# Kernel optimization log

Measured on AMD Instinct MI355X. Metric: run time of the kernel, lower is better.

Reference implementation:

```python
import jax, jax.numpy as jnp
import numpy as np
from jax.ops import segment_sum

N = 100000   # nodes
E = 1600000  # edges
F = 128      # node feature dim
H = 128      # hidden dim
FE = 16      # edge feature dim
G = 256      # num graphs
EPS = 1e-5   # batch-norm eps


def setup_inputs() -> dict:
    key = jax.random.key(0)
    ks = jax.random.split(key, 16)
    s = 0.05
    return {
        "x": jax.random.normal(ks[0], (N, F), jnp.float32),
        "edge_index": jax.random.randint(ks[1], (2, E), 0, N, dtype=jnp.int32),
        "edge_attr": jax.random.normal(ks[2], (E, FE), jnp.float32),
        "batch_idx": jnp.sort(jax.random.randint(ks[3], (N,), 0, G, dtype=jnp.int32)),
        # GCN layer 1
        "W_g1": jax.random.normal(ks[4], (F, H), jnp.float32) * s,
        "b_g1": jnp.zeros((H,), jnp.float32),
        "gamma1": jnp.ones((H,), jnp.float32),
        "beta1": jnp.zeros((H,), jnp.float32),
        # GCN layer 2
        "W_g2": jax.random.normal(ks[5], (H, H), jnp.float32) * s,
        "b_g2": jnp.zeros((H,), jnp.float32),
        "gamma2": jnp.ones((H,), jnp.float32),
        "beta2": jnp.zeros((H,), jnp.float32),
        # edge encoder MLP
        "W_e1": jax.random.normal(ks[6], (FE, H), jnp.float32) * s,
        "b_e1": jnp.zeros((H,), jnp.float32),
        "W_e2": jax.random.normal(ks[7], (H, H), jnp.float32) * s,
        "b_e2": jnp.zeros((H,), jnp.float32),
    }


def _gcn_bn_relu(x, src, dst, W, b, gamma, beta):
    """GCNConv (sym-normalized, self-loops) + BatchNorm1d (batch stats) + ReLU."""
    h = x @ W                                             # [N, H]
    ones = jnp.ones((E,), h.dtype)
    deg = segment_sum(ones, dst, num_segments=N) + 1.0    # self-loop degree
    dinv = jax.lax.rsqrt(deg)                             # [N]
    norm = dinv[src] * dinv[dst]                          # [E]
    agg = segment_sum(h[src] * norm[:, None], dst, num_segments=N)
    out = agg + h * (dinv * dinv)[:, None] + b            # self-loop + bias
    mu = out.mean(axis=0)
    var = out.var(axis=0)
    out = (out - mu) * jax.lax.rsqrt(var + EPS) * gamma + beta
    return jax.nn.relu(out)


def reference(x, edge_index, edge_attr, batch_idx, W_g1, b_g1, gamma1, beta1,
              W_g2, b_g2, gamma2, beta2, W_e1, b_e1, W_e2, b_e2):
    src, dst = edge_index[0], edge_index[1]
    h = _gcn_bn_relu(x, src, dst, W_g1, b_g1, gamma1, beta1)
    h = _gcn_bn_relu(h, src, dst, W_g2, b_g2, gamma2, beta2)

    # global mean pool over nodes per graph
    node_cnt = segment_sum(jnp.ones((N,), h.dtype), batch_idx, num_segments=G)
    graph_repr = segment_sum(h, batch_idx, num_segments=G) / jnp.maximum(node_cnt, 1.0)[:, None]

    # edge encoder MLP + per-graph edge mean (vectorized version of the loop)
    e = jax.nn.relu(edge_attr @ W_e1 + b_e1) @ W_e2 + b_e2   # [E, H]
    edge_batch = batch_idx[src]                              # [E]
    edge_cnt = segment_sum(jnp.ones((E,), e.dtype), edge_batch, num_segments=G)
    edge_sum = segment_sum(e, edge_batch, num_segments=G)
    edge_repr = jnp.where(edge_cnt[:, None] > 0, edge_sum / jnp.maximum(edge_cnt, 1.0)[:, None], 0.0)

    return graph_repr + edge_repr  # [G, H]
```

## Files before the change

### kernel.cpp

```cpp
#include <hip/hip_runtime.h>
#include <cstdint>

__device__ inline unsigned int bfpack2(float a, float b) {
  unsigned int ua = __float_as_uint(a), ub = __float_as_uint(b);
  ua += 0x7FFFu + ((ua >> 16) & 1u);
  ub += 0x7FFFu + ((ub >> 16) & 1u);
  return (ua >> 16) | (ub & 0xFFFF0000u);
}
__device__ inline float bflo(unsigned int u) { return __uint_as_float(u << 16); }
__device__ inline float bfhi(unsigned int u) { return __uint_as_float(u & 0xFFFF0000u); }

__global__ __launch_bounds__(256) void pre_kernel(const int* __restrict__ src,
                                                  const int* __restrict__ dst,
                                                  int* __restrict__ deg,
                                                  int* __restrict__ deg2, int nE) {
  int e = blockIdx.x * 256 + threadIdx.x;
  if (e < nE) {
    atomicAdd(&deg[dst[e]], 1);
    atomicAdd(&deg2[src[e]], 1);
  }
}

__global__ __launch_bounds__(256) void scanA_kernel(const int* __restrict__ deg,
                                                    const int* __restrict__ deg2,
                                                    int* __restrict__ rp,
                                                    int* __restrict__ rp2,
                                                    int* __restrict__ part,
                                                    int* __restrict__ part2,
                                                    int n, int nb) {
  __shared__ int sh[256];
  int b = blockIdx.x, t = threadIdx.x;
  const int* d = (b < nb) ? deg : deg2;
  int* r = (b < nb) ? rp : rp2;
  int* p = (b < nb) ? part : part2;
  int pad = (b < nb) ? 1 : 0;
  int bb = (b < nb) ? b : b - nb;
  int base = bb * 1024 + t * 4;
  int v0 = (base + 0 < n) ? d[base + 0] : 0;
  int v1 = (base + 1 < n) ? d[base + 1] : 0;
  int v2 = (base + 2 < n) ? d[base + 2] : 0;
  int v3 = (base + 3 < n) ? d[base + 3] : 0;
  if (pad) {
    v0 = (v0 + 7) & ~7; v1 = (v1 + 7) & ~7;
    v2 = (v2 + 7) & ~7; v3 = (v3 + 7) & ~7;
  }
  int ts = v0 + v1 + v2 + v3;
  sh[t] = ts;
  __syncthreads();
  for (int off = 1; off < 256; off <<= 1) {
    int x = (t >= off) ? sh[t - off] : 0;
    __syncthreads();
    sh[t] += x;
    __syncthreads();
  }
  int excl = sh[t] - ts;
  if (t == 255) p[bb] = sh[255];
  if (base + 0 < n) r[base + 0] = excl;
  if (base + 1 < n) r[base + 1] = excl + v0;
  if (base + 2 < n) r[base + 2] = excl + v0 + v1;
  if (base + 3 < n) r[base + 3] = excl + v0 + v1 + v2;
}

__global__ void scanB_kernel(int* part, int* part2, int* rp, int* rp2, int nb, int n) {
  if (threadIdx.x == 0) {
    int* p = (blockIdx.x == 0) ? part : part2;
    int* r = (blockIdx.x == 0) ? rp : rp2;
    int run = 0;
    for (int i = 0; i < nb; ++i) { int v = p[i]; p[i] = run; run += v; }
    r[n] = run;
  }
}

__global__ __launch_bounds__(256) void scanC_kernel(int* __restrict__ rp,
                                                    int* __restrict__ rp2,
                                                    const int* __restrict__ part,
                                                    const int* __restrict__ part2,
                                                    int* __restrict__ cursor,
                                                    int* __restrict__ cursor2,
                                                    const int* __restrict__ deg,
                                                    float* __restrict__ dinv, int n) {
  int i = blockIdx.x * 256 + threadIdx.x;
  if (i < n) {
    int v = rp[i] + part[i >> 10];
    rp[i] = v;
    cursor[i] = v;
    dinv[i] = rsqrtf((float)deg[i] + 1.0f);
  } else if (i < 2 * n) {
    int j = i - n;
    int v = rp2[j] + part2[j >> 10];
    rp2[j] = v;
    cursor2[j] = v;
  }
}

__global__ __launch_bounds__(256) void placepad_kernel(const int* __restrict__ src,
                                                       const int* __restrict__ dst,
                                                       const int* __restrict__ batch,
                                                       const float* __restrict__ dinv,
                                                       int* __restrict__ cursor,
                                                       int* __restrict__ cursor2,
                                                       int2* __restrict__ swv,
                                                       unsigned int* __restrict__ epk,
                                                       const int* __restrict__ rp,
                                                       const int* __restrict__ deg,
                                                       int nE, int nN) {
  int t = blockIdx.x * 256 + threadIdx.x;
  if (t < nE) {
    int s = src[t];
    int d = dst[t];
    int p1 = atomicAdd(&cursor[d], 1);
    int2 sw; sw.x = s; sw.y = __float_as_int(dinv[s] * dinv[d]);
    swv[p1] = sw;
    int g = batch[s];
    int p2 = atomicAdd(&cursor2[s], 1);
    epk[p2] = ((unsigned int)g << 21) | (unsigned int)t;
  } else if (t < nE + nN) {
    int i = t - nE;
    int b = rp[i] + deg[i], e = rp[i + 1];
    int2 z; z.x = i; z.y = 0;
    for (int k = b; k < e; ++k) swv[k] = z;
  }
}

template <bool FUSED>
__global__ __launch_bounds__(256) void gemm128_kernel(const float* __restrict__ A,
                                                      const float* __restrict__ W,
                                                      const float* __restrict__ scale,
                                                      const float* __restrict__ shift,
                                                      unsigned int* __restrict__ hpk2,
                                                      int nrows) {
  extern __shared__ float lds[];
  float* Ws = lds;
  float* xs = lds + 128 * 128;
  const int t = threadIdx.x;
  for (int i = t; i < (128 * 128) / 4; i += 256)
    reinterpret_cast<float4*>(Ws)[i] = reinterpret_cast<const float4*>(W)[i];
  const int wave = t >> 6, lane = t & 63;
  const size_t sbase = (size_t)(lane >> 3) * (size_t)nrows * 8 + (lane & 7);
  for (int rb = blockIdx.x * 16; rb < nrows; rb += gridDim.x * 16) {
    int nr = min(16, nrows - rb);
    __syncthreads();
    for (int i = t; i < nr * 32; i += 256) {
      float4 v = reinterpret_cast<const float4*>(A + (size_t)rb * 128)[i];
      if (FUSED) {
        float4 sc4 = reinterpret_cast<const float4*>(scale)[i & 31];
        float4 sh4 = reinterpret_cast<const float4*>(shift)[i & 31];
        v.x = fmaxf(fmaf(v.x, sc4.x, sh4.x), 0.f);
        v.y = fmaxf(fmaf(v.y, sc4.y, sh4.y), 0.f);
        v.z = fmaxf(fmaf(v.z, sc4.z, sh4.z), 0.f);
        v.w = fmaxf(fmaf(v.w, sc4.w, sh4.w), 0.f);
      }
      reinterpret_cast<float4*>(xs)[i] = v;
    }
    __syncthreads();
    float acc[4][2] = {{0.f, 0.f}, {0.f, 0.f}, {0.f, 0.f}, {0.f, 0.f}};
    const float* xw = xs + wave * 4 * 128;
#pragma unroll 4
    for (int k = 0; k < 128; ++k) {
      float w0 = Ws[k * 128 + lane];
      float w1 = Ws[k * 128 + 64 + lane];
#pragma unroll
      for (int r = 0; r < 4; ++r) {
        float a = xw[r * 128 + k];
        acc[r][0] = fmaf(a, w0, acc[r][0]);
        acc[r][1] = fmaf(a, w1, acc[r][1]);
      }
    }
#pragma unroll
    for (int r = 0; r < 4; ++r) {
      int row = rb + wave * 4 + r;
      if (row < nrows)
        hpk2[sbase + (size_t)row * 8] = bfpack2(acc[r][0], acc[r][1]);
    }
  }
}

__global__ __launch_bounds__(256) void spmm8_kernel(const unsigned int* __restrict__ hpk2,
                                                    const float* __restrict__ dinv,
                                                    const int* __restrict__ rp,
                                                    const int2* __restrict__ swv,
                                                    const float* __restrict__ bias,
                                                    float* __restrict__ outp,
                                                    float* __restrict__ bnsum,
                                                    float* __restrict__ bnsq, int nN) {
  const int lane = threadIdx.x & 63;
  const int ch = lane & 7;
  const int es = lane >> 3;
  const int slice = blockIdx.x & 7;
  const unsigned int* hs = hpk2 + (size_t)slice * (size_t)nN * 8;
  const int cb = slice * 8;
  const int wib = (int)(blockIdx.x >> 3) * 4 + (int)(threadIdx.x >> 6);
  const int nws = (int)(gridDim.x >> 3) * 4;
  const unsigned long long* swq = reinterpret_cast<const unsigned long long*>(swv);
  float b0 = bias[cb + ch], b1 = bias[64 + cb + ch];
  float s0 = 0.f, s1 = 0.f, q0 = 0.f, q1 = 0.f;
  for (int n = wib; n < nN; n += nws) {
    const int beg = rp[n], end = rp[n + 1];
    float a0 = 0.f, a1 = 0.f, c0 = 0.f, c1 = 0.f;
    int j = beg;
    for (; j + 8 < end; j += 16) {
      unsigned long long v0 = __builtin_nontemporal_load(swq + j + es);
      unsigned long long v1 = __builtin_nontemporal_load(swq + j + 8 + es);
      int sA = (int)(unsigned int)v0;
      int sB = (int)(unsigned int)v1;
      float wA = __uint_as_float((unsigned int)(v0 >> 32));
      float wB = __uint_as_float((unsigned int)(v1 >> 32));
      unsigned int pA = hs[(size_t)sA * 8 + ch];
      unsigned int pB = hs[(size_t)sB * 8 + ch];
      a0 = fmaf(wA, bflo(pA), a0); a1 = fmaf(wA, bfhi(pA), a1);
      c0 = fmaf(wB, bflo(pB), c0); c1 = fmaf(wB, bfhi(pB), c1);
    }
    if (j < end) {
      unsigned long long v0 = __builtin_nontemporal_load(swq + j + es);
      int sA = (int)(unsigned int)v0;
      float wA = __uint_as_float((unsigned int)(v0 >> 32));
      unsigned int pA = hs[(size_t)sA * 8 + ch];
      a0 = fmaf(wA, bflo(pA), a0); a1 = fmaf(wA, bfhi(pA), a1);
    }
    a0 += c0; a1 += c1;
    a0 += __shfl_xor(a0, 8);  a1 += __shfl_xor(a1, 8);
    a0 += __shfl_xor(a0, 16); a1 += __shfl_xor(a1, 16);
    a0 += __shfl_xor(a0, 32); a1 += __shfl_xor(a1, 32);
    if (es == 0) {
      float dn = dinv[n];
      float sw = dn * dn;
      unsigned int pn = hs[(size_t)n * 8 + ch];
      float o0 = fmaf(bflo(pn), sw, a0) + b0;
      float o1 = fmaf(bfhi(pn), sw, a1) + b1;
      __builtin_nontemporal_store(o0, &outp[(size_t)n * 128 + cb + ch]);
      __builtin_nontemporal_store(o1, &outp[(size_t)n * 128 + 64 + cb + ch]);
      s0 += o0; s1 += o1;
      q0 = fmaf(o0, o0, q0); q1 = fmaf(o1, o1, q1);
    }
  }
  if (es == 0) {
    atomicAdd(&bnsum[cb + ch], s0);
    atomicAdd(&bnsum[64 + cb + ch], s1);
    atomicAdd(&bnsq[cb + ch], q0);
    atomicAdd(&bnsq[64 + cb + ch], q1);
  }
}

__global__ void bnfin_kernel(const float* __restrict__ sum, const float* __restrict__ sq,
                             const float* __restrict__ gamma, const float* __restrict__ beta,
                             float* __restrict__ scale, float* __restrict__ shift,
                             float invN) {
  int c = threadIdx.x;
  float mu = sum[c] * invN;
  float var = sq[c] * invN - mu * mu;
  float sc = gamma[c] * rsqrtf(var + 1e-5f);
  scale[c] = sc;
  shift[c] = beta[c] - mu * sc;
}

__global__ __launch_bounds__(256) void pool_kernel(const float* __restrict__ h,
                                                   const int* __restrict__ batch,
                                                   const float* __restrict__ scale,
                                                   const float* __restrict__ shift,
                                                   float* __restrict__ gsum,
                                                   float* __restrict__ gcnt,
                                                   int nN, int chunk) {
  const int lane = threadIdx.x & 63;
  const int wid = (blockIdx.x * blockDim.x + threadIdx.x) >> 6;
  int beg = wid * chunk;
  if (beg >= nN) return;
  int end = min(nN, beg + chunk);
  const int c2 = 2 * lane;
  float2 sc2 = *reinterpret_cast<const float2*>(scale + c2);
  float2 sh2 = *reinterpret_cast<const float2*>(shift + c2);
  int cur = -1;
  float a0 = 0.f, a1 = 0.f, cnt = 0.f;
  for (int n = beg; n < end; ++n) {
    int g = batch[n];
    if (g != cur) {
      if (cur >= 0) {
        atomicAdd(&gsum[cur * 128 + c2], a0);
        atomicAdd(&gsum[cur * 128 + c2 + 1], a1);
        if (lane == 0) atomicAdd(&gcnt[cur], cnt);
      }
      cur = g; a0 = 0.f; a1 = 0.f; cnt = 0.f;
    }
    float2 v = *reinterpret_cast<const float2*>(h + (size_t)n * 128 + c2);
    a0 += fmaxf(fmaf(v.x, sc2.x, sh2.x), 0.f);
    a1 += fmaxf(fmaf(v.y, sc2.y, sh2.y), 0.f);
    cnt += 1.f;
  }
  if (cur >= 0) {
    atomicAdd(&gsum[cur * 128 + c2], a0);
    atomicAdd(&gsum[cur * 128 + c2 + 1], a1);
    if (lane == 0) atomicAdd(&gcnt[cur], cnt);
  }
}

__global__ __launch_bounds__(256) void edge2_kernel(const float* __restrict__ ea,
                                                    const unsigned int* __restrict__ epk,
                                                    const float* __restrict__ We1,
                                                    const float* __restrict__ be1,
                                                    float* __restrict__ esum,
                                                    float* __restrict__ ecnt,
                                                    int nE, int chunk) {
  const int lane = threadIdx.x & 63;
  const int wid = (blockIdx.x * 256 + threadIdx.x) >> 6;
  int beg = wid * chunk;
  if (beg >= nE) return;
  int end = min(nE, beg + chunk);
  float w0[16], w1[16];
#pragma unroll
  for (int k = 0; k < 16; ++k) {
    w0[k] = We1[k * 128 + lane];
    w1[k] = We1[k * 128 + 64 + lane];
  }
  float b0 = be1[lane], b1 = be1[64 + lane];
  int cur = -1;
  float a0 = 0.f, a1 = 0.f, cnt = 0.f;
  for (int j = beg; j < end; ++j) {
    unsigned int pk = epk[j];
    int g = (int)(pk >> 21);
    int e = (int)(pk & 0x1FFFFFu);
    if (g != cur) {
      if (cur >= 0) {
        atomicAdd(&esum[cur * 128 + lane], a0);
        atomicAdd(&esum[cur * 128 + 64 + lane], a1);
        if (lane == 0) atomicAdd(&ecnt[cur], cnt);
      }
      cur = g; a0 = 0.f; a1 = 0.f; cnt = 0.f;
    }
    const float4* eap = reinterpret_cast<const float4*>(ea + (size_t)e * 16);
    float4 t0 = eap[0], t1 = eap[1], t2 = eap[2], t3 = eap[3];
    float u0 = b0, u1 = b1;
    u0 = fmaf(t0.x, w0[0], u0);  u1 = fmaf(t0.x, w1[0], u1);
    u0 = fmaf(t0.y, w0[1], u0);  u1 = fmaf(t0.y, w1[1], u1);
    u0 = fmaf(t0.z, w0[2], u0);  u1 = fmaf(t0.z, w1[2], u1);
    u0 = fmaf(t0.w, w0[3], u0);  u1 = fmaf(t0.w, w1[3], u1);
    u0 = fmaf(t1.x, w0[4], u0);  u1 = fmaf(t1.x, w1[4], u1);
    u0 = fmaf(t1.y, w0[5], u0);  u1 = fmaf(t1.y, w1[5], u1);
    u0 = fmaf(t1.z, w0[6], u0);  u1 = fmaf(t1.z, w1[6], u1);
    u0 = fmaf(t1.w, w0[7], u0);  u1 = fmaf(t1.w, w1[7], u1);
    u0 = fmaf(t2.x, w0[8], u0);  u1 = fmaf(t2.x, w1[8], u1);
    u0 = fmaf(t2.y, w0[9], u0);  u1 = fmaf(t2.y, w1[9], u1);
    u0 = fmaf(t2.z, w0[10], u0); u1 = fmaf(t2.z, w1[10], u1);
    u0 = fmaf(t2.w, w0[11], u0); u1 = fmaf(t2.w, w1[11], u1);
    u0 = fmaf(t3.x, w0[12], u0); u1 = fmaf(t3.x, w1[12], u1);
    u0 = fmaf(t3.y, w0[13], u0); u1 = fmaf(t3.y, w1[13], u1);
    u0 = fmaf(t3.z, w0[14], u0); u1 = fmaf(t3.z, w1[14], u1);
    u0 = fmaf(t3.w, w0[15], u0); u1 = fmaf(t3.w, w1[15], u1);
    a0 += fmaxf(u0, 0.f);
    a1 += fmaxf(u1, 0.f);
    cnt += 1.f;
  }
  if (cur >= 0) {
    atomicAdd(&esum[cur * 128 + lane], a0);
    atomicAdd(&esum[cur * 128 + 64 + lane], a1);
    if (lane == 0) atomicAdd(&ecnt[cur], cnt);
  }
}

__global__ __launch_bounds__(128) void final_kernel(const float* __restrict__ gsum,
                                                    const float* __restrict__ gcnt,
                                                    const float* __restrict__ esum,
                                                    const float* __restrict__ ecnt,
                                                    const float* __restrict__ We2,
                                                    const float* __restrict__ be2,
                                                    float* __restrict__ out) {
  __shared__ float row[128];
  int g = blockIdx.x, c = threadIdx.x;
  row[c] = esum[g * 128 + c];
  __syncthreads();
  float acc = 0.f;
#pragma unroll 4
  for (int k = 0; k < 128; ++k) acc = fmaf(row[k], We2[k * 128 + c], acc);
  float ce = ecnt[g];
  float er = (ce > 0.f) ? (acc / ce + be2[c]) : 0.f;
  float cn = gcnt[g];
  float gr = gsum[g * 128 + c] / fmaxf(cn, 1.f);
  out[g * 128 + c] = gr + er;
}

extern "C" void kernel_launch(void* const* d_in, const int* in_sizes, int n_in,
                              void* d_out, int out_size, void* d_ws, size_t ws_size,
                              hipStream_t stream) {
  const float* x    = (const float*)d_in[0];
  const int*   ei   = (const int*)d_in[1];
  const float* ea   = (const float*)d_in[2];
  const int*   bidx = (const int*)d_in[3];
  const float* Wg1  = (const float*)d_in[4];
  const float* bg1  = (const float*)d_in[5];
  const float* gm1  = (const float*)d_in[6];
  const float* bt1  = (const float*)d_in[7];
  const float* Wg2  = (const float*)d_in[8];
  const float* bg2  = (const float*)d_in[9];
  const float* gm2  = (const float*)d_in[10];
  const float* bt2  = (const float*)d_in[11];
  const float* We1  = (const float*)d_in[12];
  const float* be1  = (const float*)d_in[13];
  const float* We2  = (const float*)d_in[14];
  const float* be2  = (const float*)d_in[15];
  float* out = (float*)d_out;

  const int N = in_sizes[3];
  const int E = in_sizes[1] / 2;
  const int G = out_size / 128;
  const int* srcp = ei;
  const int* dstp = ei + E;
  const int Epad = E + 8 * N;

  char* w = (char*)d_ws;
  auto alloc = [&](size_t b) {
    char* p = w;
    w += (b + 15) & ~(size_t)15;
    return p;
  };
  float* bufB    = (float*)alloc((size_t)N * 128 * 4);
  unsigned int* hpk2 = (unsigned int*)alloc((size_t)N * 64 * 4);
  int2*  swv     = (int2*)alloc((size_t)Epad * 8);
  unsigned int* epk = (unsigned int*)alloc((size_t)E * 4);
  int*   rp      = (int*)alloc((size_t)(N + 1) * 4);
  int*   rp2     = (int*)alloc((size_t)(N + 1) * 4);
  int*   cursor  = (int*)alloc((size_t)N * 4);
  int*   cursor2 = (int*)alloc((size_t)N * 4);
  float* dinv    = (float*)alloc((size_t)N * 4);
  char* zbase = w;
  int*   deg  = (int*)alloc((size_t)N * 4);
  int*   deg2 = (int*)alloc((size_t)N * 4);
  float* bs1  = (float*)alloc(512);
  float* bq1  = (float*)alloc(512);
  float* bs2  = (float*)alloc(512);
  float* bq2  = (float*)alloc(512);
  float* gsum = (float*)alloc((size_t)G * 128 * 4);
  float* gcnt = (float*)alloc((size_t)G * 4);
  float* esum = (float*)alloc((size_t)G * 128 * 4);
  float* ecnt = (float*)alloc((size_t)G * 4);
  int*   part  = (int*)alloc(4096);
  int*   part2 = (int*)alloc(4096);
  size_t zbytes = (size_t)(w - zbase);
  float* sc1 = (float*)alloc(512);
  float* sh1 = (float*)alloc(512);
  float* sc2 = (float*)alloc(512);
  float* sh2 = (float*)alloc(512);

  hipMemsetAsync(zbase, 0, zbytes, stream);

  (void)hipFuncSetAttribute((const void*)gemm128_kernel<false>,
                            hipFuncAttributeMaxDynamicSharedMemorySize, 73728);
  (void)hipFuncSetAttribute((const void*)gemm128_kernel<true>,
                            hipFuncAttributeMaxDynamicSharedMemorySize, 73728);

  pre_kernel<<<(E + 255) / 256, 256, 0, stream>>>(srcp, dstp, deg, deg2, E);
  int nb = (N + 1023) / 1024;
  scanA_kernel<<<2 * nb, 256, 0, stream>>>(deg, deg2, rp, rp2, part, part2, N, nb);
  scanB_kernel<<<2, 64, 0, stream>>>(part, part2, rp, rp2, nb, N);
  scanC_kernel<<<(2 * N + 255) / 256, 256, 0, stream>>>(rp, rp2, part, part2, cursor,
                                                        cursor2, deg, dinv, N);
  placepad_kernel<<<(E + N + 255) / 256, 256, 0, stream>>>(srcp, dstp, bidx, dinv, cursor,
                                                           cursor2, swv, epk, rp, deg, E, N);

  gemm128_kernel<false><<<512, 256, 73728, stream>>>(x, Wg1, nullptr, nullptr, hpk2, N);
  spmm8_kernel<<<2048, 256, 0, stream>>>(hpk2, dinv, rp, swv, bg1, bufB, bs1, bq1, N);
  bnfin_kernel<<<1, 128, 0, stream>>>(bs1, bq1, gm1, bt1, sc1, sh1, 1.0f / (float)N);

  gemm128_kernel<true><<<512, 256, 73728, stream>>>(bufB, Wg2, sc1, sh1, hpk2, N);
  spmm8_kernel<<<2048, 256, 0, stream>>>(hpk2, dinv, rp, swv, bg2, bufB, bs2, bq2, N);
  bnfin_kernel<<<1, 128, 0, stream>>>(bs2, bq2, gm2, bt2, sc2, sh2, 1.0f / (float)N);

  int nwp = (2048 * 256) / 64;
  int chunkN = (N + nwp - 1) / nwp;
  pool_kernel<<<2048, 256, 0, stream>>>(bufB, bidx, sc2, sh2, gsum, gcnt, N, chunkN);
  int nwe = (2048 * 256) / 64;
  int chunkE = (E + nwe - 1) / nwe;
  edge2_kernel<<<2048, 256, 0, stream>>>(ea, epk, We1, be1, esum, ecnt, E, chunkE);
  final_kernel<<<G, 128, 0, stream>>>(gsum, gcnt, esum, ecnt, We2, be2, out);
}
```

Before: 1.336 ms.

## Drop source-sorted edge CSR; accumulate edge means in LDS; pair nodes in SpMM

Removes the second CSR build (source degrees, second scan, cursor2, epk placement) that only served the edge encoder. The edge encoder now streams edges in their original order, looks up each edge's graph through src and batch, and accumulates per-graph sums in a full 256x128 LDS table using shared atomics. Each block writes that table to a per-block partial buffer that aliases hpk2, and final_kernel reduces the 256 partials. Separately, the SpMM kernel processes two nodes per wave iteration to expose more independent gathers, at the cost of more registers and uneven tail handling.

After: 1.969 ms. 47.3% more time.

```diff
diff --git a/kernel.cpp b/kernel.cpp
--- a/kernel.cpp
+++ b/kernel.cpp
@@ -10,40 +10,24 @@
 __device__ inline float bflo(unsigned int u) { return __uint_as_float(u << 16); }
 __device__ inline float bfhi(unsigned int u) { return __uint_as_float(u & 0xFFFF0000u); }
 
-__global__ __launch_bounds__(256) void pre_kernel(const int* __restrict__ src,
-                                                  const int* __restrict__ dst,
-                                                  int* __restrict__ deg,
-                                                  int* __restrict__ deg2, int nE) {
+__global__ __launch_bounds__(256) void pre_kernel(const int* __restrict__ dst,
+                                                  int* __restrict__ deg, int nE) {
   int e = blockIdx.x * 256 + threadIdx.x;
-  if (e < nE) {
-    atomicAdd(&deg[dst[e]], 1);
-    atomicAdd(&deg2[src[e]], 1);
-  }
+  if (e < nE) atomicAdd(&deg[dst[e]], 1);
 }
 
 __global__ __launch_bounds__(256) void scanA_kernel(const int* __restrict__ deg,
-                                                    const int* __restrict__ deg2,
                                                     int* __restrict__ rp,
-                                                    int* __restrict__ rp2,
-                                                    int* __restrict__ part,
-                                                    int* __restrict__ part2,
-                                                    int n, int nb) {
+                                                    int* __restrict__ part, int n) {
   __shared__ int sh[256];
   int b = blockIdx.x, t = threadIdx.x;
-  const int* d = (b < nb) ? deg : deg2;
-  int* r = (b < nb) ? rp : rp2;
-  int* p = (b < nb) ? part : part2;
-  int pad = (b < nb) ? 1 : 0;
-  int bb = (b < nb) ? b : b - nb;
-  int base = bb * 1024 + t * 4;
-  int v0 = (base + 0 < n) ? d[base + 0] : 0;
-  int v1 = (base + 1 < n) ? d[base + 1] : 0;
-  int v2 = (base + 2 < n) ? d[base + 2] : 0;
-  int v3 = (base + 3 < n) ? d[base + 3] : 0;
-  if (pad) {
-    v0 = (v0 + 7) & ~7; v1 = (v1 + 7) & ~7;
-    v2 = (v2 + 7) & ~7; v3 = (v3 + 7) & ~7;
-  }
+  int base = b * 1024 + t * 4;
+  int v0 = (base + 0 < n) ? deg[base + 0] : 0;
+  int v1 = (base + 1 < n) ? deg[base + 1] : 0;
+  int v2 = (base + 2 < n) ? deg[base + 2] : 0;
+  int v3 = (base + 3 < n) ? deg[base + 3] : 0;
+  v0 = (v0 + 7) & ~7; v1 = (v1 + 7) & ~7;
+  v2 = (v2 + 7) & ~7; v3 = (v3 + 7) & ~7;
   int ts = v0 + v1 + v2 + v3;
   sh[t] = ts;
   __syncthreads();
@@ -54,29 +38,24 @@
     __syncthreads();
   }
   int excl = sh[t] - ts;
-  if (t == 255) p[bb] = sh[255];
-  if (base + 0 < n) r[base + 0] = excl;
-  if (base + 1 < n) r[base + 1] = excl + v0;
-  if (base + 2 < n) r[base + 2] = excl + v0 + v1;
-  if (base + 3 < n) r[base + 3] = excl + v0 + v1 + v2;
-}
-
-__global__ void scanB_kernel(int* part, int* part2, int* rp, int* rp2, int nb, int n) {
-  if (threadIdx.x == 0) {
-    int* p = (blockIdx.x == 0) ? part : part2;
-    int* r = (blockIdx.x == 0) ? rp : rp2;
+  if (t == 255) part[b] = sh[255];
+  if (base + 0 < n) rp[base + 0] = excl;
+  if (base + 1 < n) rp[base + 1] = excl + v0;
+  if (base + 2 < n) rp[base + 2] = excl + v0 + v1;
+  if (base + 3 < n) rp[base + 3] = excl + v0 + v1 + v2;
+}
+
+__global__ void scanB_kernel(int* part, int* rp, int nb, int n) {
+  if (blockIdx.x == 0 && threadIdx.x == 0) {
     int run = 0;
-    for (int i = 0; i < nb; ++i) { int v = p[i]; p[i] = run; run += v; }
-    r[n] = run;
+    for (int i = 0; i < nb; ++i) { int v = part[i]; part[i] = run; run += v; }
+    rp[n] = run;
   }
 }
 
 __global__ __launch_bounds__(256) void scanC_kernel(int* __restrict__ rp,
-                                                    int* __restrict__ rp2,
                                                     const int* __restrict__ part,
-                                                    const int* __restrict__ part2,
                                                     int* __restrict__ cursor,
-                                                    int* __restrict__ cursor2,
                                                     const int* __restrict__ deg,
                                                     float* __restrict__ dinv, int n) {
   int i = blockIdx.x * 256 + threadIdx.x;
@@ -85,22 +64,14 @@
     rp[i] = v;
     cursor[i] = v;
     dinv[i] = rsqrtf((float)deg[i] + 1.0f);
-  } else if (i < 2 * n) {
-    int j = i - n;
-    int v = rp2[j] + part2[j >> 10];
-    rp2[j] = v;
-    cursor2[j] = v;
   }
 }
 
 __global__ __launch_bounds__(256) void placepad_kernel(const int* __restrict__ src,
                                                        const int* __restrict__ dst,
-                                                       const int* __restrict__ batch,
                                                        const float* __restrict__ dinv,
                                                        int* __restrict__ cursor,
-                                                       int* __restrict__ cursor2,
                                                        int2* __restrict__ swv,
-                                                       unsigned int* __restrict__ epk,
                                                        const int* __restrict__ rp,
                                                        const int* __restrict__ deg,
                                                        int nE, int nN) {
@@ -111,9 +82,6 @@
     int p1 = atomicAdd(&cursor[d], 1);
     int2 sw; sw.x = s; sw.y = __float_as_int(dinv[s] * dinv[d]);
     swv[p1] = sw;
-    int g = batch[s];
-    int p2 = atomicAdd(&cursor2[s], 1);
-    epk[p2] = ((unsigned int)g << 21) | (unsigned int)t;
   } else if (t < nE + nN) {
     int i = t - nE;
     int b = rp[i] + deg[i], e = rp[i + 1];
@@ -194,45 +162,81 @@
   const unsigned long long* swq = reinterpret_cast<const unsigned long long*>(swv);
   float b0 = bias[cb + ch], b1 = bias[64 + cb + ch];
   float s0 = 0.f, s1 = 0.f, q0 = 0.f, q1 = 0.f;
-  for (int n = wib; n < nN; n += nws) {
-    const int beg = rp[n], end = rp[n + 1];
-    float a0 = 0.f, a1 = 0.f, c0 = 0.f, c1 = 0.f;
-    int j = beg;
-    for (; j + 8 < end; j += 16) {
-      unsigned long long v0 = __builtin_nontemporal_load(swq + j + es);
-      unsigned long long v1 = __builtin_nontemporal_load(swq + j + 8 + es);
-      int sA = (int)(unsigned int)v0;
-      int sB = (int)(unsigned int)v1;
-      float wA = __uint_as_float((unsigned int)(v0 >> 32));
-      float wB = __uint_as_float((unsigned int)(v1 >> 32));
-      unsigned int pA = hs[(size_t)sA * 8 + ch];
-      unsigned int pB = hs[(size_t)sB * 8 + ch];
-      a0 = fmaf(wA, bflo(pA), a0); a1 = fmaf(wA, bfhi(pA), a1);
-      c0 = fmaf(wB, bflo(pB), c0); c1 = fmaf(wB, bfhi(pB), c1);
-    }
-    if (j < end) {
-      unsigned long long v0 = __builtin_nontemporal_load(swq + j + es);
-      int sA = (int)(unsigned int)v0;
-      float wA = __uint_as_float((unsigned int)(v0 >> 32));
-      unsigned int pA = hs[(size_t)sA * 8 + ch];
-      a0 = fmaf(wA, bflo(pA), a0); a1 = fmaf(wA, bfhi(pA), a1);
-    }
-    a0 += c0; a1 += c1;
-    a0 += __shfl_xor(a0, 8);  a1 += __shfl_xor(a1, 8);
-    a0 += __shfl_xor(a0, 16); a1 += __shfl_xor(a1, 16);
-    a0 += __shfl_xor(a0, 32); a1 += __shfl_xor(a1, 32);
+  const int half = (nN + 1) >> 1;
+
+#define SPMM_CHUNK(J, ACC0, ACC1)                                         \
+  {                                                                       \
+    unsigned long long v_ = __builtin_nontemporal_load(swq + (J) + es);   \
+    unsigned int pp_ = hs[(size_t)(unsigned int)v_ * 8 + ch];             \
+    float ww_ = __uint_as_float((unsigned int)(v_ >> 32));                \
+    ACC0 = fmaf(ww_, bflo(pp_), ACC0);                                    \
+    ACC1 = fmaf(ww_, bfhi(pp_), ACC1);                                    \
+  }
+
+  for (int p = wib; p < half; p += nws) {
+    const int n0 = p;
+    const int n1 = p + half;
+    const bool has1 = n1 < nN;
+    int j0 = rp[n0];
+    const int end0 = rp[n0 + 1];
+    int j1 = 0, end1 = 0;
+    if (has1) { j1 = rp[n1]; end1 = rp[n1 + 1]; }
+    float a00 = 0.f, a01 = 0.f, b00 = 0.f, b01 = 0.f;
+    float a10 = 0.f, a11 = 0.f, b10 = 0.f, b11 = 0.f;
+    while (j0 + 8 < end0 && j1 + 8 < end1) {
+      SPMM_CHUNK(j0, a00, a01);
+      SPMM_CHUNK(j0 + 8, b00, b01);
+      SPMM_CHUNK(j1, a10, a11);
+      SPMM_CHUNK(j1 + 8, b10, b11);
+      j0 += 16; j1 += 16;
+    }
+    while (j0 + 8 < end0) {
+      SPMM_CHUNK(j0, a00, a01);
+      SPMM_CHUNK(j0 + 8, b00, b01);
+      j0 += 16;
+    }
+    if (j0 < end0) SPMM_CHUNK(j0, a00, a01);
+    while (j1 + 8 < end1) {
+      SPMM_CHUNK(j1, a10, a11);
+      SPMM_CHUNK(j1 + 8, b10, b11);
+      j1 += 16;
+    }
+    if (j1 < end1) SPMM_CHUNK(j1, a10, a11);
+
+    a00 += b00; a01 += b01;
+    a10 += b10; a11 += b11;
+    a00 += __shfl_xor(a00, 8);  a01 += __shfl_xor(a01, 8);
+    a10 += __shfl_xor(a10, 8);  a11 += __shfl_xor(a11, 8);
+    a00 += __shfl_xor(a00, 16); a01 += __shfl_xor(a01, 16);
+    a10 += __shfl_xor(a10, 16); a11 += __shfl_xor(a11, 16);
+    a00 += __shfl_xor(a00, 32); a01 += __shfl_xor(a01, 32);
+    a10 += __shfl_xor(a10, 32); a11 += __shfl_xor(a11, 32);
     if (es == 0) {
-      float dn = dinv[n];
-      float sw = dn * dn;
-      unsigned int pn = hs[(size_t)n * 8 + ch];
-      float o0 = fmaf(bflo(pn), sw, a0) + b0;
-      float o1 = fmaf(bfhi(pn), sw, a1) + b1;
-      __builtin_nontemporal_store(o0, &outp[(size_t)n * 128 + cb + ch]);
-      __builtin_nontemporal_store(o1, &outp[(size_t)n * 128 + 64 + cb + ch]);
-      s0 += o0; s1 += o1;
-      q0 = fmaf(o0, o0, q0); q1 = fmaf(o1, o1, q1);
-    }
-  }
+      {
+        float dn = dinv[n0];
+        float sw = dn * dn;
+        unsigned int pn = hs[(size_t)n0 * 8 + ch];
+        float o0 = fmaf(bflo(pn), sw, a00) + b0;
+        float o1 = fmaf(bfhi(pn), sw, a01) + b1;
+        __builtin_nontemporal_store(o0, &outp[(size_t)n0 * 128 + cb + ch]);
+        __builtin_nontemporal_store(o1, &outp[(size_t)n0 * 128 + 64 + cb + ch]);
+        s0 += o0; s1 += o1;
+        q0 = fmaf(o0, o0, q0); q1 = fmaf(o1, o1, q1);
+      }
+      if (has1) {
+        float dn = dinv[n1];
+        float sw = dn * dn;
+        unsigned int pn = hs[(size_t)n1 * 8 + ch];
+        float o0 = fmaf(bflo(pn), sw, a10) + b0;
+        float o1 = fmaf(bfhi(pn), sw, a11) + b1;
+        __builtin_nontemporal_store(o0, &outp[(size_t)n1 * 128 + cb + ch]);
+        __builtin_nontemporal_store(o1, &outp[(size_t)n1 * 128 + 64 + cb + ch]);
+        s0 += o0; s1 += o1;
+        q0 = fmaf(o0, o0, q0); q1 = fmaf(o1, o1, q1);
+      }
+    }
+  }
+#undef SPMM_CHUNK
   if (es == 0) {
     atomicAdd(&bnsum[cb + ch], s0);
     atomicAdd(&bnsum[64 + cb + ch], s1);
@@ -292,18 +296,18 @@
   }
 }
 
-__global__ __launch_bounds__(256) void edge2_kernel(const float* __restrict__ ea,
-                                                    const unsigned int* __restrict__ epk,
-                                                    const float* __restrict__ We1,
-                                                    const float* __restrict__ be1,
-                                                    float* __restrict__ esum,
-                                                    float* __restrict__ ecnt,
-                                                    int nE, int chunk) {
-  const int lane = threadIdx.x & 63;
-  const int wid = (blockIdx.x * 256 + threadIdx.x) >> 6;
-  int beg = wid * chunk;
-  if (beg >= nE) return;
-  int end = min(nE, beg + chunk);
+__global__ __launch_bounds__(1024) void edge3_kernel(const float* __restrict__ ea,
+                                                     const int* __restrict__ src,
+                                                     const int* __restrict__ batch,
+                                                     const float* __restrict__ We1,
+                                                     const float* __restrict__ be1,
+                                                     float* __restrict__ pb,
+                                                     int nE, int chunk) {
+  extern __shared__ float es[];
+  float* cs = es + 256 * 128;
+  const int t = threadIdx.x;
+  for (int i = t; i < 256 * 128 + 256; i += 1024) es[i] = 0.f;
+  const int lane = t & 63;
   float w0[16], w1[16];
 #pragma unroll
   for (int k = 0; k < 16; ++k) {
@@ -311,68 +315,86 @@
     w1[k] = We1[k * 128 + 64 + lane];
   }
   float b0 = be1[lane], b1 = be1[64 + lane];
-  int cur = -1;
-  float a0 = 0.f, a1 = 0.f, cnt = 0.f;
-  for (int j = beg; j < end; ++j) {
-    unsigned int pk = epk[j];
-    int g = (int)(pk >> 21);
-    int e = (int)(pk & 0x1FFFFFu);
-    if (g != cur) {
-      if (cur >= 0) {
-        atomicAdd(&esum[cur * 128 + lane], a0);
-        atomicAdd(&esum[cur * 128 + 64 + lane], a1);
-        if (lane == 0) atomicAdd(&ecnt[cur], cnt);
-      }
-      cur = g; a0 = 0.f; a1 = 0.f; cnt = 0.f;
-    }
-    const float4* eap = reinterpret_cast<const float4*>(ea + (size_t)e * 16);
-    float4 t0 = eap[0], t1 = eap[1], t2 = eap[2], t3 = eap[3];
-    float u0 = b0, u1 = b1;
-    u0 = fmaf(t0.x, w0[0], u0);  u1 = fmaf(t0.x, w1[0], u1);
-    u0 = fmaf(t0.y, w0[1], u0);  u1 = fmaf(t0.y, w1[1], u1);
-    u0 = fmaf(t0.z, w0[2], u0);  u1 = fmaf(t0.z, w1[2], u1);
-    u0 = fmaf(t0.w, w0[3], u0);  u1 = fmaf(t0.w, w1[3], u1);
-    u0 = fmaf(t1.x, w0[4], u0);  u1 = fmaf(t1.x, w1[4], u1);
-    u0 = fmaf(t1.y, w0[5], u0);  u1 = fmaf(t1.y, w1[5], u1);
-    u0 = fmaf(t1.z, w0[6], u0);  u1 = fmaf(t1.z, w1[6], u1);
-    u0 = fmaf(t1.w, w0[7], u0);  u1 = fmaf(t1.w, w1[7], u1);
-    u0 = fmaf(t2.x, w0[8], u0);  u1 = fmaf(t2.x, w1[8], u1);
-    u0 = fmaf(t2.y, w0[9], u0);  u1 = fmaf(t2.y, w1[9], u1);
-    u0 = fmaf(t2.z, w0[10], u0); u1 = fmaf(t2.z, w1[10], u1);
-    u0 = fmaf(t2.w, w0[11], u0); u1 = fmaf(t2.w, w1[11], u1);
-    u0 = fmaf(t3.x, w0[12], u0); u1 = fmaf(t3.x, w1[12], u1);
-    u0 = fmaf(t3.y, w0[13], u0); u1 = fmaf(t3.y, w1[13], u1);
-    u0 = fmaf(t3.z, w0[14], u0); u1 = fmaf(t3.z, w1[14], u1);
-    u0 = fmaf(t3.w, w0[15], u0); u1 = fmaf(t3.w, w1[15], u1);
-    a0 += fmaxf(u0, 0.f);
-    a1 += fmaxf(u1, 0.f);
-    cnt += 1.f;
-  }
-  if (cur >= 0) {
-    atomicAdd(&esum[cur * 128 + lane], a0);
-    atomicAdd(&esum[cur * 128 + 64 + lane], a1);
-    if (lane == 0) atomicAdd(&ecnt[cur], cnt);
-  }
+  __syncthreads();
+  const int wid = (blockIdx.x * 1024 + t) >> 6;
+  int beg = wid * chunk;
+  int end = min(nE, beg + chunk);
+  if (beg < end) {
+    int e = beg;
+    for (; e + 1 < end; e += 2) {
+      int s0 = src[e], s1 = src[e + 1];
+      int g0 = batch[s0], g1 = batch[s1];
+      const float4* p0 = reinterpret_cast<const float4*>(ea + (size_t)e * 16);
+      float4 A0 = p0[0], A1 = p0[1], A2 = p0[2], A3 = p0[3];
+      float4 B0 = p0[4], B1 = p0[5], B2 = p0[6], B3 = p0[7];
+      float av[16] = {A0.x, A0.y, A0.z, A0.w, A1.x, A1.y, A1.z, A1.w,
+                      A2.x, A2.y, A2.z, A2.w, A3.x, A3.y, A3.z, A3.w};
+      float bv[16] = {B0.x, B0.y, B0.z, B0.w, B1.x, B1.y, B1.z, B1.w,
+                      B2.x, B2.y, B2.z, B2.w, B3.x, B3.y, B3.z, B3.w};
+      float u0 = b0, u1 = b1, x0 = b0, x1 = b1;
+#pragma unroll
+      for (int k = 0; k < 16; ++k) {
+        u0 = fmaf(av[k], w0[k], u0);
+        u1 = fmaf(av[k], w1[k], u1);
+        x0 = fmaf(bv[k], w0[k], x0);
+        x1 = fmaf(bv[k], w1[k], x1);
+      }
+      u0 = fmaxf(u0, 0.f); u1 = fmaxf(u1, 0.f);
+      x0 = fmaxf(x0, 0.f); x1 = fmaxf(x1, 0.f);
+      atomicAdd(&es[g0 * 128 + lane], u0);
+      atomicAdd(&es[g0 * 128 + 64 + lane], u1);
+      atomicAdd(&es[g1 * 128 + lane], x0);
+      atomicAdd(&es[g1 * 128 + 64 + lane], x1);
+      if (lane == 0) {
+        atomicAdd(&cs[g0], 1.f);
+        atomicAdd(&cs[g1], 1.f);
+      }
+    }
+    if (e < end) {
+      int s0 = src[e];
+      int g0 = batch[s0];
+      const float4* p0 = reinterpret_cast<const float4*>(ea + (size_t)e * 16);
+      float4 A0 = p0[0], A1 = p0[1], A2 = p0[2], A3 = p0[3];
+      float av[16] = {A0.x, A0.y, A0.z, A0.w, A1.x, A1.y, A1.z, A1.w,
+                      A2.x, A2.y, A2.z, A2.w, A3.x, A3.y, A3.z, A3.w};
+      float u0 = b0, u1 = b1;
+#pragma unroll
+      for (int k = 0; k < 16; ++k) {
+        u0 = fmaf(av[k], w0[k], u0);
+        u1 = fmaf(av[k], w1[k], u1);
+      }
+      u0 = fmaxf(u0, 0.f); u1 = fmaxf(u1, 0.f);
+      atomicAdd(&es[g0 * 128 + lane], u0);
+      atomicAdd(&es[g0 * 128 + 64 + lane], u1);
+      if (lane == 0) atomicAdd(&cs[g0], 1.f);
+    }
+  }
+  __syncthreads();
+  float* myp = pb + (size_t)blockIdx.x * 33024;
+  for (int i = t; i < 256 * 128 + 256; i += 1024) myp[i] = es[i];
 }
 
 __global__ __launch_bounds__(128) void final_kernel(const float* __restrict__ gsum,
                                                     const float* __restrict__ gcnt,
-                                                    const float* __restrict__ esum,
-                                                    const float* __restrict__ ecnt,
+                                                    const float* __restrict__ pb,
                                                     const float* __restrict__ We2,
                                                     const float* __restrict__ be2,
                                                     float* __restrict__ out) {
   __shared__ float row[128];
   int g = blockIdx.x, c = threadIdx.x;
-  row[c] = esum[g * 128 + c];
+  float acc_e = 0.f, cnt_e = 0.f;
+  for (int b = 0; b < 256; ++b) {
+    const float* base = pb + (size_t)b * 33024;
+    acc_e += base[g * 128 + c];
+    cnt_e += base[256 * 128 + g];
+  }
+  row[c] = acc_e;
   __syncthreads();
   float acc = 0.f;
 #pragma unroll 4
   for (int k = 0; k < 128; ++k) acc = fmaf(row[k], We2[k * 128 + c], acc);
-  float ce = ecnt[g];
-  float er = (ce > 0.f) ? (acc / ce + be2[c]) : 0.f;
-  float cn = gcnt[g];
-  float gr = gsum[g * 128 + c] / fmaxf(cn, 1.f);
+  float er = (cnt_e > 0.f) ? (acc / cnt_e + be2[c]) : 0.f;
+  float gr = gsum[g * 128 + c] / fmaxf(gcnt[g], 1.f);
   out[g * 128 + c] = gr + er;
 }
 
@@ -413,46 +435,42 @@
   float* bufB    = (float*)alloc((size_t)N * 128 * 4);
   unsigned int* hpk2 = (unsigned int*)alloc((size_t)N * 64 * 4);
   int2*  swv     = (int2*)alloc((size_t)Epad * 8);
-  unsigned int* epk = (unsigned int*)alloc((size_t)E * 4);
   int*   rp      = (int*)alloc((size_t)(N + 1) * 4);
-  int*   rp2     = (int*)alloc((size_t)(N + 1) * 4);
   int*   cursor  = (int*)alloc((size_t)N * 4);
-  int*   cursor2 = (int*)alloc((size_t)N * 4);
   float* dinv    = (float*)alloc((size_t)N * 4);
   char* zbase = w;
   int*   deg  = (int*)alloc((size_t)N * 4);
-  int*   deg2 = (int*)alloc((size_t)N * 4);
   float* bs1  = (float*)alloc(512);
   float* bq1  = (float*)alloc(512);
   float* bs2  = (float*)alloc(512);
   float* bq2  = (float*)alloc(512);
   float* gsum = (float*)alloc((size_t)G * 128 * 4);
   float* gcnt = (float*)alloc((size_t)G * 4);
-  float* esum = (float*)alloc((size_t)G * 128 * 4);
-  float* ecnt = (float*)alloc((size_t)G * 4);
-  int*   part  = (int*)alloc(4096);
-  int*   part2 = (int*)alloc(4096);
+  int*   part = (int*)alloc(4096);
   size_t zbytes = (size_t)(w - zbase);
   float* sc1 = (float*)alloc(512);
   float* sh1 = (float*)alloc(512);
   float* sc2 = (float*)alloc(512);
   float* sh2 = (float*)alloc(512);
 
+  float* pb = (float*)hpk2;
+
   hipMemsetAsync(zbase, 0, zbytes, stream);
 
   (void)hipFuncSetAttribute((const void*)gemm128_kernel<false>,
                             hipFuncAttributeMaxDynamicSharedMemorySize, 73728);
   (void)hipFuncSetAttribute((const void*)gemm128_kernel<true>,
                             hipFuncAttributeMaxDynamicSharedMemorySize, 73728);
-
-  pre_kernel<<<(E + 255) / 256, 256, 0, stream>>>(srcp, dstp, deg, deg2, E);
+  (void)hipFuncSetAttribute((const void*)edge3_kernel,
+                            hipFuncAttributeMaxDynamicSharedMemorySize, 132096);
+
+  pre_kernel<<<(E + 255) / 256, 256, 0, stream>>>(dstp, deg, E);
   int nb = (N + 1023) / 1024;
-  scanA_kernel<<<2 * nb, 256, 0, stream>>>(deg, deg2, rp, rp2, part, part2, N, nb);
-  scanB_kernel<<<2, 64, 0, stream>>>(part, part2, rp, rp2, nb, N);
-  scanC_kernel<<<(2 * N + 255) / 256, 256, 0, stream>>>(rp, rp2, part, part2, cursor,
-                                                        cursor2, deg, dinv, N);
-  placepad_kernel<<<(E + N + 255) / 256, 256, 0, stream>>>(srcp, dstp, bidx, dinv, cursor,
-                                                           cursor2, swv, epk, rp, deg, E, N);
+  scanA_kernel<<<nb, 256, 0, stream>>>(deg, rp, part, N);
+  scanB_kernel<<<1, 1, 0, stream>>>(part, rp, nb, N);
+  scanC_kernel<<<(N + 255) / 256, 256, 0, stream>>>(rp, part, cursor, deg, dinv, N);
+  placepad_kernel<<<(E + N + 255) / 256, 256, 0, stream>>>(srcp, dstp, dinv, cursor,
+                                                           swv, rp, deg, E, N);
 
   gemm128_kernel<false><<<512, 256, 73728, stream>>>(x, Wg1, nullptr, nullptr, hpk2, N);
   spmm8_kernel<<<2048, 256, 0, stream>>>(hpk2, dinv, rp, swv, bg1, bufB, bs1, bq1, N);
@@ -465,8 +483,10 @@
   int nwp = (2048 * 256) / 64;
   int chunkN = (N + nwp - 1) / nwp;
   pool_kernel<<<2048, 256, 0, stream>>>(bufB, bidx, sc2, sh2, gsum, gcnt, N, chunkN);
-  int nwe = (2048 * 256) / 64;
-  int chunkE = (E + nwe - 1) / nwe;
-  edge2_kernel<<<2048, 256, 0, stream>>>(ea, epk, We1, be1, esum, ecnt, E, chunkE);
-  final_kernel<<<G, 128, 0, stream>>>(gsum, gcnt, esum, ecnt, We2, be2, out);
-}
+
+  int nweg = 256 * 16;
+  int chunkE = (E + nweg - 1) / nweg;
+  edge3_kernel<<<256, 1024, 132096, stream>>>(ea, srcp, bidx, We1, be1, pb, E, chunkE);
+
+  final_kernel<<<G, 128, 0, stream>>>(gsum, gcnt, pb, We2, be2, out);
+}
```
